# Kernel optimization log

Measured on AMD Instinct MI355X. Metric: run time of the kernel, lower is better.

## Reference

```python
import jax, jax.numpy as jnp
import numpy as np

B, T, V, E, H, L = 32, 128, 32000, 1024, 1024, 3


def lstm_layer(x, Wx, Wh, b, h0, c0):
    """Standard LSTM (i,f,g,o gate order). x: [B,T,D]. Returns ([B,T,H], (h,c))."""
    def step(carry, xt):
        h, c = carry
        z = xt @ Wx + h @ Wh + b          # [B, 4H]
        i, f, g, o = jnp.split(z, 4, axis=-1)
        c = jax.nn.sigmoid(f) * c + jax.nn.sigmoid(i) * jnp.tanh(g)
        h = jax.nn.sigmoid(o) * jnp.tanh(c)
        return (h, c), h
    (h, c), ys = jax.lax.scan(step, (h0, c0), jnp.swapaxes(x, 0, 1))
    return jnp.swapaxes(ys, 0, 1), (h, c)


def setup_inputs() -> dict:
    key = jax.random.key(0)
    ks = jax.random.split(key, 12)
    s = 0.05  # small init to avoid gate saturation
    inp = {
        "enc_ids": jax.random.randint(ks[0], (B, T), 0, V, dtype=jnp.int32),
        "dec_ids": jax.random.randint(ks[1], (B, T), 0, V, dtype=jnp.int32),
        "emb": jax.random.normal(ks[2], (V, E), jnp.float32) * s,
        "Wx_enc": jax.random.normal(ks[3], (L, E, 4 * H), jnp.float32) * s,
        "Wh_enc": jax.random.normal(ks[4], (L, H, 4 * H), jnp.float32) * s,
        "b_enc": jnp.zeros((L, 4 * H), jnp.float32),
        "Wx_dec": jax.random.normal(ks[5], (L, E, 4 * H), jnp.float32) * s,
        "Wh_dec": jax.random.normal(ks[6], (L, H, 4 * H), jnp.float32) * s,
        "b_dec": jnp.zeros((L, 4 * H), jnp.float32),
        "dense_W": jax.random.normal(ks[7], (H, V), jnp.float32) * s,
        "dense_b": jnp.zeros((V,), jnp.float32),
    }
    return inp


def reference(enc_ids, dec_ids, emb, Wx_enc, Wh_enc, b_enc, Wx_dec, Wh_dec, b_dec, dense_W, dense_b):
    zeros = jnp.zeros((B, H), jnp.float32)
    # encoder: 3 stacked LSTMs, zero initial state each
    x = emb[enc_ids]                                      # [B,T,E]
    state = (zeros, zeros)
    for l in range(L):
        x, state = lstm_layer(x, Wx_enc[l], Wh_enc[l], b_enc[l], zeros, zeros)
    # decoder: faithful to source state chaining:
    # dec layer0 init = enc layer2 final; dec layer_{i+1} init = dec layer_i final
    y = emb[dec_ids]                                      # [B,T,E]
    for l in range(L):
        y, state = lstm_layer(y, Wx_dec[l], Wh_dec[l], b_dec[l], state[0], state[1])
    logits = y.reshape(-1, H) @ dense_W + dense_b          # [B*T, V]
    return logits.reshape(B, T, V)
```

## Files before the change

### kernel.cpp

```cpp
#include <hip/hip_runtime.h>


typedef __bf16 bf8 __attribute__((ext_vector_type(8)));
typedef float  f4  __attribute__((ext_vector_type(4)));

#define TLEN  128
#define HID   1024
#define G4    4096
#define VOC   32000
#define NBLK_SEQ 64

__device__ __forceinline__ ushort f2bf(float f) {
  unsigned u = __builtin_bit_cast(unsigned, f);
  u += 0x7fffu + ((u >> 16) & 1u);
  return (ushort)(u >> 16);
}
__device__ __forceinline__ float sigmoidf_(float x) { return 1.f / (1.f + expf(-x)); }

__device__ __forceinline__ void ld16_sys(uint4& v, const void* p) {
  asm volatile("global_load_dwordx4 %0, %1, off sc0 sc1" : "=v"(v) : "v"(p));
}
__device__ __forceinline__ unsigned ld4_sys(const void* p) {
  unsigned v;
  asm volatile("global_load_dword %0, %1, off sc0 sc1\n\ts_waitcnt vmcnt(0)"
               : "=v"(v) : "v"(p) : "memory");
  return v;
}
__device__ __forceinline__ void ld4_sys3(unsigned& a, unsigned& b, unsigned& c,
                                         const void* pa, const void* pb, const void* pc) {
  asm volatile("global_load_dword %0, %3, off sc0 sc1\n\t"
               "global_load_dword %1, %4, off sc0 sc1\n\t"
               "global_load_dword %2, %5, off sc0 sc1\n\t"
               "s_waitcnt vmcnt(0)"
               : "=&v"(a), "=&v"(b), "=&v"(c)
               : "v"(pa), "v"(pb), "v"(pc) : "memory");
}
__device__ __forceinline__ void st4_sys(void* p, unsigned v) {
  asm volatile("global_store_dword %0, %1, off sc0 sc1" :: "v"(p), "v"(v) : "memory");
}
__device__ __forceinline__ void wait_vm0() {
  asm volatile("s_waitcnt vmcnt(0)" ::: "memory");
  __builtin_amdgcn_sched_barrier(0);
}

typedef const __attribute__((address_space(1))) void GvoidC;
typedef __attribute__((address_space(3))) void Lvoid;
__device__ __forceinline__ void g2l16(const void* g, void* l) {
  __builtin_amdgcn_global_load_lds((GvoidC*)g, (Lvoid*)l, 16, 0, 0);
}

__global__ __launch_bounds__(256) void embed_kernel(const int* __restrict__ ids,
    const float* __restrict__ emb, ushort* __restrict__ out) {
  int r = blockIdx.x;
  int b = r & 31, t = r >> 5;
  int id = ids[b * TLEN + t];
  const float4* src = (const float4*)(emb + (size_t)id * HID);
  float4 v = src[threadIdx.x];
  ushort4 o;
  o.x = f2bf(v.x); o.y = f2bf(v.y); o.z = f2bf(v.z); o.w = f2bf(v.w);
  *(ushort4*)(out + (size_t)r * HID + threadIdx.x * 4) = o;
}

__global__ __launch_bounds__(256) void transpose_cvt(const float* __restrict__ W,
    ushort* __restrict__ Wt, int R, int C) {
  __shared__ float tile[32][33];
  int tx = threadIdx.x & 31, ty = threadIdx.x >> 5;
  int c0 = blockIdx.x * 32, r0 = blockIdx.y * 32;
  #pragma unroll
  for (int i = 0; i < 32; i += 8)
    tile[ty + i][tx] = W[(size_t)(r0 + ty + i) * C + c0 + tx];
  __syncthreads();
  #pragma unroll
  for (int i = 0; i < 32; i += 8)
    Wt[(size_t)(c0 + ty + i) * R + r0 + tx] = f2bf(tile[tx][ty + i]);
}

__global__ __launch_bounds__(256) void gemm_bt(const ushort* __restrict__ A,
    const ushort* __restrict__ Bt, const float* __restrict__ bias,
    float* __restrict__ C, int M, int N, int K, int permute) {
  __shared__ __align__(16) ushort lA[128 * 32];
  __shared__ __align__(16) ushort lB[128 * 32];
  int tid = threadIdx.x;
  int lane = tid & 63, wave = tid >> 6;
  int nwg = gridDim.x * gridDim.y;
  int wg  = blockIdx.y * gridDim.x + blockIdx.x;
  int q   = nwg >> 3;
  int swg = (wg & 7) * q + (wg >> 3);
  int m0 = (swg / gridDim.x) * 128, n0 = (swg % gridDim.x) * 128;
  int wr = wave >> 1, wc = wave & 1;
  f4 zero = {0.f, 0.f, 0.f, 0.f};
  f4 acc[4][4];
  #pragma unroll
  for (int i = 0; i < 4; i++)
    #pragma unroll
    for (int j = 0; j < 4; j++) acc[i][j] = zero;

  const ushort* Ag = A  + (size_t)(m0 + wave * 32 + (lane >> 2)) * K + (lane & 3) * 8;
  const ushort* Bg = Bt + (size_t)(n0 + wave * 32 + (lane >> 2)) * K + (lane & 3) * 8;
  ushort* lAp = lA + wave * 32 * 32;
  ushort* lBp = lB + wave * 32 * 32;

  for (int kt = 0; kt < K; kt += 32) {
    g2l16(Ag + kt, lAp);
    g2l16(Ag + (size_t)16 * K + kt, lAp + 16 * 32);
    g2l16(Bg + kt, lBp);
    g2l16(Bg + (size_t)16 * K + kt, lBp + 16 * 32);
    __syncthreads();
    bf8 aF[4], bF[4];
    #pragma unroll
    for (int i = 0; i < 4; i++)
      aF[i] = *(const bf8*)(lA + (wr * 64 + i * 16 + (lane & 15)) * 32 + (lane >> 4) * 8);
    #pragma unroll
    for (int j = 0; j < 4; j++)
      bF[j] = *(const bf8*)(lB + (wc * 64 + j * 16 + (lane & 15)) * 32 + (lane >> 4) * 8);
    #pragma unroll
    for (int i = 0; i < 4; i++)
      #pragma unroll
      for (int j = 0; j < 4; j++)
        acc[i][j] = __builtin_amdgcn_mfma_f32_16x16x32_bf16(aF[i], bF[j], acc[i][j], 0, 0, 0);
    __syncthreads();
  }
  #pragma unroll
  for (int i = 0; i < 4; i++) {
    #pragma unroll
    for (int j = 0; j < 4; j++) {
      int col = n0 + wc * 64 + j * 16 + (lane & 15);
      float bv = bias ? bias[col] : 0.f;
      #pragma unroll
      for (int v = 0; v < 4; v++) {
        int row = m0 + wr * 64 + i * 16 + (lane >> 4) * 4 + v;
        int orow = permute ? ((row & 31) * TLEN + (row >> 5)) : row;
        C[(size_t)orow * N + col] = acc[i][j][v] + bv;
      }
    }
  }
}

__global__ __launch_bounds__(512, 1) void enc_wave(
    const float*  __restrict__ Zpre,
    const ushort* __restrict__ WhT,
    const ushort* __restrict__ WxT,
    const float*  __restrict__ bE,
    ushort*       __restrict__ hxe,
    float*        __restrict__ cSe,
    ushort*       __restrict__ hS,
    unsigned*     __restrict__ flags)
{
  const int bx = blockIdx.x;
  const int l = bx >> 6, jg = bx & 63;
  const int j0 = jg * 16;
  const int tid = threadIdx.x;
  const int lane = tid & 63, wave = tid >> 6;
  const int g = wave & 3, op = wave >> 2;
  const int rr = tid >> 4, jj = tid & 15;

  __shared__ __align__(16) char hLDS[65536];
  __shared__ __align__(16) char xLDS[65536];
  __shared__ float zbuf[8][32][17];

  float cc = cSe[(size_t)l * 32768 + rr * HID + j0 + jj];
  float bias4[4];
  #pragma unroll
  for (int gg = 0; gg < 4; gg++)
    bias4[gg] = bE[l * G4 + gg * HID + j0 + jj];

  const bool mfma_on = (l > 0) || (op == 0);
  bf8 bw[32];
  if (mfma_on) {
    const ushort* Wb = op ? (WxT + (size_t)(l - 1) * G4 * HID)
                          : (WhT + (size_t)l * G4 * HID);
    const ushort* Bp = Wb + (size_t)(g * HID + j0 + (lane & 15)) * HID + (lane >> 4) * 8;
    #pragma unroll
    for (int kk = 0; kk < 32; kk++) bw[kk] = *(const bf8*)(Bp + kk * 32);
  }

  const int r0 = lane & 15, r1 = r0 + 16;
  const int klb = (lane >> 4) * 16;
  const int swz = (r0 & 7) << 4;

  float zv4[4], zn4[4];
  if (l == 0) {
    #pragma unroll
    for (int gg = 0; gg < 4; gg++)
      zv4[gg] = Zpre[(size_t)rr * G4 + gg * HID + j0 + jj];
  }

  for (int w = 0; w < 130; ++w) {
    if (w > 0) {
      if (wave == 0) {
        for (;;) {
          unsigned a, b, c;
          ld4_sys3(a, b, c, flags + lane * 4, flags + (64 + lane) * 4,
                   flags + (128 + lane) * 4);
          if (!__ballot(a < (unsigned)w || b < (unsigned)w || c < (unsigned)w)) break;
          __builtin_amdgcn_s_sleep(1);
        }
      }
      __syncthreads();
    }
    const int t = w - l;
    if (t >= 0 && t < TLEN) {
      const char* hsrc = (const char*)(hxe + ((size_t)l * 2 + ((t - 1) & 1)) * 32768);
      uint4 hreg[8], xreg[8];
      #pragma unroll
      for (int it = 0; it < 8; it++)
        ld16_sys(hreg[it], hsrc + (size_t)(tid + it * 512) * 16);
      if (l > 0) {
        const char* xsrc = (const char*)(hxe + ((size_t)(l - 1) * 2 + (t & 1)) * 32768);
        #pragma unroll
        for (int it = 0; it < 8; it++)
          ld16_sys(xreg[it], xsrc + (size_t)(tid + it * 512) * 16);
      }
      wait_vm0();
      #pragma unroll
      for (int it = 0; it < 8; it++) {
        int c = tid + it * 512;
        int row = c >> 7;
        int o = (c & 127) * 16;
        *(uint4*)(hLDS + row * 2048 + (o ^ ((row & 7) << 4))) = hreg[it];
      }
      if (l > 0) {
        #pragma unroll
        for (int it = 0; it < 8; it++) {
          int c = tid + it * 512;
          int row = c >> 7;
          int o = (c & 127) * 16;
          *(uint4*)(xLDS + row * 2048 + (o ^ ((row & 7) << 4))) = xreg[it];
        }
      }
      __syncthreads();

      if (l == 0 && t + 1 < TLEN) {
        const float* Ztn = Zpre + (size_t)(t + 1) * 32 * G4;
        #pragma unroll
        for (int gg = 0; gg < 4; gg++)
          zn4[gg] = Ztn[(size_t)rr * G4 + gg * HID + j0 + jj];
      }

      if (mfma_on) {
        const char* S = op ? xLDS : hLDS;
        f4 acc0 = {0.f, 0.f, 0.f, 0.f}, acc1 = {0.f, 0.f, 0.f, 0.f};
        #pragma unroll
        for (int kk = 0; kk < 32; kk++) {
          int cb = kk * 64 + klb;
          bf8 a0 = *(const bf8*)(S + r0 * 2048 + (cb ^ swz));
          bf8 a1 = *(const bf8*)(S + r1 * 2048 + (cb ^ swz));
          acc0 = __builtin_amdgcn_mfma_f32_16x16x32_bf16(a0, bw[kk], acc0, 0, 0, 0);
          acc1 = __builtin_amdgcn_mfma_f32_16x16x32_bf16(a1, bw[kk], acc1, 0, 0, 0);
        }
        #pragma unroll
        for (int v = 0; v < 4; v++) {
          zbuf[wave][(lane >> 4) * 4 + v][lane & 15]      = acc0[v];
          zbuf[wave][16 + (lane >> 4) * 4 + v][lane & 15] = acc1[v];
        }
      }
      __syncthreads();

      float z[4];
      #pragma unroll
      for (int gg = 0; gg < 4; gg++) z[gg] = zbuf[gg][rr][jj];
      if (l > 0) {
        #pragma unroll
        for (int gg = 0; gg < 4; gg++) z[gg] += zbuf[4 + gg][rr][jj] + bias4[gg];
      } else {
        #pragma unroll
        for (int gg = 0; gg < 4; gg++) z[gg] += zv4[gg];
        #pragma unroll
        for (int gg = 0; gg < 4; gg++) zv4[gg] = zn4[gg];
      }
      float ig = sigmoidf_(z[0]), fg = sigmoidf_(z[1]);
      float gv = tanhf(z[2]),     og = sigmoidf_(z[3]);
      cc = fg * cc + ig * gv;
      float hv = og * tanhf(cc);
      ushort hb = f2bf(hv);
      unsigned u = (unsigned)hb;
      unsigned nb = __shfl_xor(u, 1);
      if ((jj & 1) == 0)
        st4_sys(hxe + ((size_t)l * 2 + (t & 1)) * 32768 + rr * HID + j0 + jj,
                u | (nb << 16));
      if (t == TLEN - 1) {
        hS [(size_t)l * 32768 + rr * HID + j0 + jj] = hb;
        cSe[(size_t)l * 32768 + rr * HID + j0 + jj] = cc;
      }
      wait_vm0();
    }
    __syncthreads();
    if (tid == 0) st4_sys(flags + bx * 4, (unsigned)(w + 1));
  }
}

__global__ __launch_bounds__(256, 1) void lstm_seq(
    const float*  __restrict__ Zpre,
    const ushort* __restrict__ Wht,
    const ushort* __restrict__ h0,
    float*        __restrict__ cS,
    ushort*       __restrict__ yout,
    unsigned*     __restrict__ flags)
{
  const int jg = blockIdx.x;
  const int j0 = jg * 16;
  const int tid = threadIdx.x;
  const int lane = tid & 63, wave = tid >> 6;
  const int rr = tid >> 3, cp = tid & 7;

  __shared__ __align__(16) char hLDS[65536];
  __shared__ float zp[4][4][32][17];

  float2 cc = *(const float2*)(cS + (size_t)rr * HID + j0 + 2 * cp);

  bf8 bw[4][8];
  #pragma unroll
  for (int g = 0; g < 4; g++) {
    const ushort* Bp = Wht + (size_t)(g * HID + j0 + (lane & 15)) * HID
                     + wave * 256 + (lane >> 4) * 8;
    #pragma unroll
    for (int kk = 0; kk < 8; kk++)
      bw[g][kk] = *(const bf8*)(Bp + kk * 32);
  }

  const int r0 = lane & 15, r1 = r0 + 16;
  const int klb = (lane >> 4) * 16;
  const int swz = (r0 & 7) << 4;
  const int kbase = wave * 512;

  float2 zv[4], zn[4];
  #pragma unroll
  for (int g = 0; g < 4; g++)
    zv[g] = *(const float2*)(Zpre + (size_t)rr * G4 + g * HID + j0 + 2 * cp);

  for (int t = 0; t < TLEN; ++t) {
    if (t > 0) {
      if (wave == 0) {
        const unsigned* fp = flags + lane * 4;
        while (__ballot(ld4_sys(fp) < (unsigned)t)) __builtin_amdgcn_s_sleep(1);
      }
      __syncthreads();
    }
    const char* hsrc = (t == 0) ? (const char*)h0
                                : (const char*)(yout + (size_t)(t - 1) * 32 * HID);
    uint4 hreg[16];
    #pragma unroll
    for (int it = 0; it < 16; it++)
      ld16_sys(hreg[it], hsrc + (size_t)(tid + it * 256) * 16);
    wait_vm0();
    #pragma unroll
    for (int it = 0; it < 16; it++) {
      int c = tid + it * 256;
      int row = c >> 7;
      int o = (c & 127) * 16;
      *(uint4*)(hLDS + row * 2048 + (o ^ ((row & 7) << 4))) = hreg[it];
    }
    __syncthreads();

    if (t + 1 < TLEN) {
      const float* Ztn = Zpre + (size_t)(t + 1) * 32 * G4;
      #pragma unroll
      for (int g = 0; g < 4; g++)
        zn[g] = *(const float2*)(Ztn + (size_t)rr * G4 + g * HID + j0 + 2 * cp);
    }

    f4 acc0[4], acc1[4];
    #pragma unroll
    for (int g = 0; g < 4; g++) { acc0[g] = (f4){0,0,0,0}; acc1[g] = (f4){0,0,0,0}; }
    #pragma unroll
    for (int kk = 0; kk < 8; kk++) {
      int cb = kbase + kk * 64 + klb;
      bf8 a0 = *(const bf8*)(hLDS + r0 * 2048 + (cb ^ swz));
      bf8 a1 = *(const bf8*)(hLDS + r1 * 2048 + (cb ^ swz));
      #pragma unroll
      for (int g = 0; g < 4; g++) {
        acc0[g] = __builtin_amdgcn_mfma_f32_16x16x32_bf16(a0, bw[g][kk], acc0[g], 0, 0, 0);
        acc1[g] = __builtin_amdgcn_mfma_f32_16x16x32_bf16(a1, bw[g][kk], acc1[g], 0, 0, 0);
      }
    }
    #pragma unroll
    for (int g = 0; g < 4; g++)
      #pragma unroll
      for (int v = 0; v < 4; v++) {
        zp[wave][g][(lane >> 4) * 4 + v][lane & 15]      = acc0[g][v];
        zp[wave][g][16 + (lane >> 4) * 4 + v][lane & 15] = acc1[g][v];
      }
    __syncthreads();

    float zx[4], zy[4];
    #pragma unroll
    for (int g = 0; g < 4; g++) {
      zx[g] = zv[g].x + zp[0][g][rr][2 * cp]     + zp[1][g][rr][2 * cp]
                      + zp[2][g][rr][2 * cp]     + zp[3][g][rr][2 * cp];
      zy[g] = zv[g].y + zp[0][g][rr][2 * cp + 1] + zp[1][g][rr][2 * cp + 1]
                      + zp[2][g][rr][2 * cp + 1] + zp[3][g][rr][2 * cp + 1];
    }
    cc.x = sigmoidf_(zx[1]) * cc.x + sigmoidf_(zx[0]) * tanhf(zx[2]);
    cc.y = sigmoidf_(zy[1]) * cc.y + sigmoidf_(zy[0]) * tanhf(zy[2]);
    float hv0 = sigmoidf_(zx[3]) * tanhf(cc.x);
    float hv1 = sigmoidf_(zy[3]) * tanhf(cc.y);
    unsigned packed = (unsigned)f2bf(hv0) | ((unsigned)f2bf(hv1) << 16);
    st4_sys((char*)(yout + (size_t)t * 32 * HID) + ((size_t)rr * HID + j0 + 2 * cp) * 2,
            packed);
    #pragma unroll
    for (int g = 0; g < 4; g++) zv[g] = zn[g];

    wait_vm0();
    __syncthreads();
    if (tid == 0) st4_sys(flags + jg * 4, (unsigned)(t + 1));
  }
  *(float2*)(cS + (size_t)rr * HID + j0 + 2 * cp) = cc;
}

__global__ __launch_bounds__(256) void prep_enc(ushort* hxe, float* cSe,
                                                unsigned* flags) {
  int i = blockIdx.x * 256 + threadIdx.x;
  hxe[i] = 0;
  if (i < 98304) cSe[i] = 0.f;
  if (i < 192)   flags[i * 4] = 0;
}
__global__ __launch_bounds__(256) void prep_dec0(const ushort* __restrict__ hS2,
                                                 const float* __restrict__ cSe2,
                                                 ushort* h0, float* cS,
                                                 unsigned* flags) {
  int i = blockIdx.x * 256 + threadIdx.x;
  h0[i] = hS2[i];
  cS[i] = cSe2[i];
  if (i < NBLK_SEQ) flags[i * 4] = 0;
}
__global__ __launch_bounds__(256) void prep_copy(const ushort* __restrict__ src,
                                                 ushort* __restrict__ h0,
                                                 unsigned* __restrict__ flags) {
  int i = blockIdx.x * 256 + threadIdx.x;
  h0[i] = src[i];
  if (i < NBLK_SEQ) flags[i * 4] = 0;
}

extern "C" void kernel_launch(void* const* d_in, const int* in_sizes, int n_in,
                              void* d_out, int out_size, void* d_ws, size_t ws_size,
                              hipStream_t stream) {
  const int*   enc_ids = (const int*)d_in[0];
  const int*   dec_ids = (const int*)d_in[1];
  const float* emb     = (const float*)d_in[2];
  const float* Wx_enc  = (const float*)d_in[3];
  const float* Wh_enc  = (const float*)d_in[4];
  const float* b_enc   = (const float*)d_in[5];
  const float* Wx_dec  = (const float*)d_in[6];
  const float* Wh_dec  = (const float*)d_in[7];
  const float* b_dec   = (const float*)d_in[8];
  const float* dense_W = (const float*)d_in[9];
  const float* dense_b = (const float*)d_in[10];
  float* out = (float*)d_out;

  char* ws = (char*)d_ws;
  const size_t SZ_BUF = (size_t)4096 * 1024 * 2;
  ushort*   bufA   = (ushort*)(ws);
  ushort*   bufB   = (ushort*)(ws + SZ_BUF);
  ushort*   Wxt    = (ushort*)(ws + 2 * SZ_BUF);
  ushort*   Wht    = (ushort*)(ws + 3 * SZ_BUF);
  ushort*   dWt    = (ushort*)(ws + 4 * SZ_BUF);
  char*     p2     = ws + 4 * SZ_BUF + (size_t)VOC * 1024 * 2;
  ushort*   hstate = (ushort*)p2;
  float*    cS     = (float*)(p2 + (size_t)32 * 1024 * 2);
  unsigned* flags  = (unsigned*)(p2 + (size_t)32 * 1024 * 2 + (size_t)32 * 1024 * 4);

  char* ob = (char*)d_out;
  float*    Zpre   = out;
  ushort*   WhTe   = (ushort*)(ob + (size_t)64  * 1024 * 1024);
  ushort*   WxTe   = (ushort*)(ob + (size_t)88  * 1024 * 1024);
  char*     st     = ob + (size_t)112 * 1024 * 1024;
  ushort*   hxe    = (ushort*)st;
  float*    cSe    = (float*)(st + 393216);
  ushort*   hS     = (ushort*)(st + 786432);
  unsigned* flags2 = (unsigned*)(st + 983040);
  const size_t WSTRIDE = (size_t)G4 * HID;

  transpose_cvt<<<dim3(VOC / 32, 1024 / 32), 256, 0, stream>>>(dense_W, dWt, 1024, VOC);

  embed_kernel<<<4096, 256, 0, stream>>>(enc_ids, emb, bufA);
  transpose_cvt<<<dim3(G4 / 32, 32), 256, 0, stream>>>(Wx_enc, Wxt, 1024, G4);
  gemm_bt<<<dim3(G4 / 128, 4096 / 128), 256, 0, stream>>>(bufA, Wxt, b_enc,
                                                          Zpre, 4096, G4, 1024, 0);
  for (int l = 0; l < 3; l++)
    transpose_cvt<<<dim3(G4 / 32, 32), 256, 0, stream>>>(Wh_enc + (size_t)l * 1024 * G4,
                                                         WhTe + l * WSTRIDE, 1024, G4);
  for (int l = 1; l < 3; l++)
    transpose_cvt<<<dim3(G4 / 32, 32), 256, 0, stream>>>(Wx_enc + (size_t)l * 1024 * G4,
                                                         WxTe + (l - 1) * WSTRIDE, 1024, G4);
  prep_enc<<<768, 256, 0, stream>>>(hxe, cSe, flags2);
  enc_wave<<<192, 512, 0, stream>>>(Zpre, WhTe, WxTe, b_enc, hxe, cSe, hS, flags2);

  embed_kernel<<<4096, 256, 0, stream>>>(dec_ids, emb, bufA);
  ushort* cur = bufA; ushort* oth = bufB;
  for (int l = 0; l < 3; l++) {
    transpose_cvt<<<dim3(G4 / 32, 32), 256, 0, stream>>>(Wx_dec + (size_t)l * 1024 * G4, Wxt, 1024, G4);
    transpose_cvt<<<dim3(G4 / 32, 32), 256, 0, stream>>>(Wh_dec + (size_t)l * 1024 * G4, Wht, 1024, G4);
    gemm_bt<<<dim3(G4 / 128, 4096 / 128), 256, 0, stream>>>(cur, Wxt, b_dec + (size_t)l * G4,
                                                            Zpre, 4096, G4, 1024, 0);
    if (l == 0) {
      prep_dec0<<<128, 256, 0, stream>>>(hS + 2 * 32768, cSe + 2 * 32768, hstate, cS, flags);
    } else {
      const ushort* h0src = cur + (size_t)127 * 32 * HID;
      prep_copy<<<128, 256, 0, stream>>>(h0src, hstate, flags);
    }
    lstm_seq<<<NBLK_SEQ, 256, 0, stream>>>(Zpre, Wht, hstate, cS, oth, flags);
    ushort* tmp = cur; cur = oth; oth = tmp;
  }

  gemm_bt<<<dim3(VOC / 128, 4096 / 128), 256, 0, stream>>>(cur, dWt, dense_b, out,
                                                           4096, VOC, 1024, 1);
}
```

Baseline: 3.601 ms.

## Exchange decoder hidden state via MFMA-fragment layout, skipping LDS staging

The decoder LSTM kernel now publishes each step's hidden state into a double-buffered exchange buffer laid out in 16-column tiles. Each wave can then load its MFMA A-operand fragments straight from global memory into registers, and the full 64KB LDS copy with its extra barrier is removed. The per-step critical path through the cross-block recurrence gets shorter. The cost is a second store per step, plain rather than system-scope stores for the output sequence, and a reshuffled initial-state layout in the prep kernels.

```diff
diff --git a/kernel.cpp b/kernel.cpp
--- a/kernel.cpp
+++ b/kernel.cpp
@@ -292,9 +292,9 @@
 __global__ __launch_bounds__(256, 1) void lstm_seq(
     const float*  __restrict__ Zpre,
     const ushort* __restrict__ Wht,
-    const ushort* __restrict__ h0,
     float*        __restrict__ cS,
     ushort*       __restrict__ yout,
+    ushort*       __restrict__ hx,
     unsigned*     __restrict__ flags)
 {
   const int jg = blockIdx.x;
@@ -303,7 +303,6 @@
   const int lane = tid & 63, wave = tid >> 6;
   const int rr = tid >> 3, cp = tid & 7;
 
-  __shared__ __align__(16) char hLDS[65536];
   __shared__ float zp[4][4][32][17];
 
   float2 cc = *(const float2*)(cS + (size_t)rr * HID + j0 + 2 * cp);
@@ -319,9 +318,9 @@
   }
 
   const int r0 = lane & 15, r1 = r0 + 16;
-  const int klb = (lane >> 4) * 16;
-  const int swz = (r0 & 7) << 4;
-  const int kbase = wave * 512;
+  const int lk = lane >> 4;
+  const int aoff0 = wave * 8192 + (lk >> 1) * 512 + r0 * 16 + (lk & 1) * 8;
+  const int aoff1 = wave * 8192 + (lk >> 1) * 512 + r1 * 16 + (lk & 1) * 8;
 
   float2 zv[4], zn[4];
   #pragma unroll
@@ -336,21 +335,14 @@
       }
       __syncthreads();
     }
-    const char* hsrc = (t == 0) ? (const char*)h0
-                                : (const char*)(yout + (size_t)(t - 1) * 32 * HID);
-    uint4 hreg[16];
-    #pragma unroll
-    for (int it = 0; it < 16; it++)
-      ld16_sys(hreg[it], hsrc + (size_t)(tid + it * 256) * 16);
+    const ushort* hsrc = hx + ((t + 1) & 1) * 32768;
+    uint4 ha0[8], ha1[8];
+    #pragma unroll
+    for (int kk = 0; kk < 8; kk++) {
+      ld16_sys(ha0[kk], hsrc + aoff0 + kk * 1024);
+      ld16_sys(ha1[kk], hsrc + aoff1 + kk * 1024);
+    }
     wait_vm0();
-    #pragma unroll
-    for (int it = 0; it < 16; it++) {
-      int c = tid + it * 256;
-      int row = c >> 7;
-      int o = (c & 127) * 16;
-      *(uint4*)(hLDS + row * 2048 + (o ^ ((row & 7) << 4))) = hreg[it];
-    }
-    __syncthreads();
 
     if (t + 1 < TLEN) {
       const float* Ztn = Zpre + (size_t)(t + 1) * 32 * G4;
@@ -364,9 +356,8 @@
     for (int g = 0; g < 4; g++) { acc0[g] = (f4){0,0,0,0}; acc1[g] = (f4){0,0,0,0}; }
     #pragma unroll
     for (int kk = 0; kk < 8; kk++) {
-      int cb = kbase + kk * 64 + klb;
-      bf8 a0 = *(const bf8*)(hLDS + r0 * 2048 + (cb ^ swz));
-      bf8 a1 = *(const bf8*)(hLDS + r1 * 2048 + (cb ^ swz));
+      bf8 a0 = __builtin_bit_cast(bf8, ha0[kk]);
+      bf8 a1 = __builtin_bit_cast(bf8, ha1[kk]);
       #pragma unroll
       for (int g = 0; g < 4; g++) {
         acc0[g] = __builtin_amdgcn_mfma_f32_16x16x32_bf16(a0, bw[g][kk], acc0[g], 0, 0, 0);
@@ -395,8 +386,8 @@
     float hv0 = sigmoidf_(zx[3]) * tanhf(cc.x);
     float hv1 = sigmoidf_(zy[3]) * tanhf(cc.y);
     unsigned packed = (unsigned)f2bf(hv0) | ((unsigned)f2bf(hv1) << 16);
-    st4_sys((char*)(yout + (size_t)t * 32 * HID) + ((size_t)rr * HID + j0 + 2 * cp) * 2,
-            packed);
+    *(unsigned*)(yout + (size_t)t * 32768 + rr * HID + j0 + 2 * cp) = packed;
+    st4_sys(hx + (size_t)(t & 1) * 32768 + jg * 512 + rr * 16 + 2 * cp, packed);
     #pragma unroll
     for (int g = 0; g < 4; g++) zv[g] = zn[g];
 
@@ -416,18 +407,20 @@
 }
 __global__ __launch_bounds__(256) void prep_dec0(const ushort* __restrict__ hS2,
                                                  const float* __restrict__ cSe2,
-                                                 ushort* h0, float* cS,
+                                                 float* cS, ushort* hx,
                                                  unsigned* flags) {
   int i = blockIdx.x * 256 + threadIdx.x;
-  h0[i] = hS2[i];
+  int row = i >> 10, col = i & 1023;
+  hx[32768 + (col >> 4) * 512 + row * 16 + (col & 15)] = hS2[i];
   cS[i] = cSe2[i];
   if (i < NBLK_SEQ) flags[i * 4] = 0;
 }
 __global__ __launch_bounds__(256) void prep_copy(const ushort* __restrict__ src,
-                                                 ushort* __restrict__ h0,
+                                                 ushort* __restrict__ hx,
                                                  unsigned* __restrict__ flags) {
   int i = blockIdx.x * 256 + threadIdx.x;
-  h0[i] = src[i];
+  int row = i >> 10, col = i & 1023;
+  hx[32768 + (col >> 4) * 512 + row * 16 + (col & 15)] = src[i];
   if (i < NBLK_SEQ) flags[i * 4] = 0;
 }
 
@@ -455,7 +448,6 @@
   ushort*   Wht    = (ushort*)(ws + 3 * SZ_BUF);
   ushort*   dWt    = (ushort*)(ws + 4 * SZ_BUF);
   char*     p2     = ws + 4 * SZ_BUF + (size_t)VOC * 1024 * 2;
-  ushort*   hstate = (ushort*)p2;
   float*    cS     = (float*)(p2 + (size_t)32 * 1024 * 2);
   unsigned* flags  = (unsigned*)(p2 + (size_t)32 * 1024 * 2 + (size_t)32 * 1024 * 4);
 
@@ -468,6 +460,7 @@
   float*    cSe    = (float*)(st + 393216);
   ushort*   hS     = (ushort*)(st + 786432);
   unsigned* flags2 = (unsigned*)(st + 983040);
+  ushort*   hxD    = (ushort*)(ob + (size_t)120 * 1024 * 1024);
   const size_t WSTRIDE = (size_t)G4 * HID;
 
   transpose_cvt<<<dim3(VOC / 32, 1024 / 32), 256, 0, stream>>>(dense_W, dWt, 1024, VOC);
@@ -493,12 +486,12 @@
     gemm_bt<<<dim3(G4 / 128, 4096 / 128), 256, 0, stream>>>(cur, Wxt, b_dec + (size_t)l * G4,
                                                             Zpre, 4096, G4, 1024, 0);
     if (l == 0) {
-      prep_dec0<<<128, 256, 0, stream>>>(hS + 2 * 32768, cSe + 2 * 32768, hstate, cS, flags);
+      prep_dec0<<<128, 256, 0, stream>>>(hS + 2 * 32768, cSe + 2 * 32768, cS, hxD, flags);
     } else {
       const ushort* h0src = cur + (size_t)127 * 32 * HID;
-      prep_copy<<<128, 256, 0, stream>>>(h0src, hstate, flags);
-    }
-    lstm_seq<<<NBLK_SEQ, 256, 0, stream>>>(Zpre, Wht, hstate, cS, oth, flags);
+      prep_copy<<<128, 256, 0, stream>>>(h0src, hxD, flags);
+    }
+    lstm_seq<<<NBLK_SEQ, 256, 0, stream>>>(Zpre, Wht, cS, oth, hxD, flags);
     ushort* tmp = cur; cur = oth; oth = tmp;
   }
 
```

Measured after the change: 3.492 ms. 3.0% less time.
